# Performance work log

Hardware: AMD Instinct MI355X
Metric: run time of the kernel (lower is better)

Reference implementation:

```python
import jax, jax.numpy as jnp
import numpy as np

N_NODES = 100000

def setup_inputs() -> dict:
    key = jax.random.key(0)
    k1, k2 = jax.random.split(key)
    x = jax.random.normal(k1, (N_NODES, 48), dtype=jnp.float32)
    edge_index = jax.random.randint(k2, (2, 1600000), 0, N_NODES, dtype=jnp.int64)
    return {"x": x, "edge_index": edge_index}

def reference(x, edge_index):
    # adj = SparseTensor.from_edge_index(edge_index): row=edge_index[0], col=edge_index[1]
    # adj.matmul(x): out[i] = sum over edges with row==i of x[col]
    row, col = edge_index[0], edge_index[1]
    x_neighbors_sum = jax.ops.segment_sum(x[col], row, num_segments=x.shape[0])  # [N, D]
    node_labels = jnp.concatenate((x, x_neighbors_sum), axis=-1)  # [N, 2D]
    return node_labels
```

## Files before the change

kernel.cpp:

```cpp
#include <hip/hip_runtime.h>


constexpr int D_IN  = 48;
constexpr int BSH   = 7;
constexpr int BNODES = 1 << BSH;
constexpr int MAXNB = 1024;
constexpr int CAPB  = 2400;
constexpr int OVF_MAX = 4096;

constexpr int PT_THREADS = 256;
constexpr int PT_ITEMS   = 32;
constexpr int PT_TILE    = PT_THREADS * PT_ITEMS;

constexpr int AG_THREADS = 512;
constexpr int AG_ITEMS   = 5;


__device__ __forceinline__ unsigned int bf16rne(float f) {
    unsigned int u = __float_as_uint(f);
    return (u + 0x7fffu + ((u >> 16) & 1u)) >> 16;
}
__device__ __forceinline__ unsigned int packbf(float a, float b) {
    return bf16rne(a) | (bf16rne(b) << 16);
}
__device__ __forceinline__ void accbf(float4& a, uint2 u) {
    a.x += __uint_as_float(u.x << 16);
    a.y += __uint_as_float(u.x & 0xffff0000u);
    a.z += __uint_as_float(u.y << 16);
    a.w += __uint_as_float(u.y & 0xffff0000u);
}
__device__ __forceinline__ void add4(float4& a, const float4& b) {
    a.x += b.x; a.y += b.y; a.z += b.z; a.w += b.w;
}


__global__ __launch_bounds__(PT_THREADS)
void prep_kernel(const int* __restrict__ row, const int* __restrict__ col,
                 int* __restrict__ gcursor, unsigned int* __restrict__ pairs,
                 int* __restrict__ ovf_cnt, uint2* __restrict__ ovf,
                 const float4* __restrict__ x4, uint4* __restrict__ x2u4,
                 float4* __restrict__ out4,
                 int n_edges, int nb, int ntiles, int n_nodes) {
    __shared__ int hist[MAXNB];
    __shared__ int offs[MAXNB];
    __shared__ int gbase[MAXNB];
    __shared__ int wsum[PT_THREADS / 64];

    int t = threadIdx.x;

    if (blockIdx.x >= ntiles) {
        int i = (blockIdx.x - ntiles) * PT_THREADS + t;
        if (i < n_nodes * 6) {
            int n = i / 6, s = i - n * 6;
            float4 v0 = x4[(size_t)n * 12 + 2 * s];
            float4 v1 = x4[(size_t)n * 12 + 2 * s + 1];
            out4[(size_t)n * 24 + 2 * s]     = v0;
            out4[(size_t)n * 24 + 2 * s + 1] = v1;
            x2u4[(size_t)n * 6 + s] =
                make_uint4(packbf(v0.x, v0.y), packbf(v0.z, v0.w),
                           packbf(v1.x, v1.y), packbf(v1.z, v1.w));
        }
        return;
    }

    int tile0 = blockIdx.x * PT_TILE;

    for (int i = t; i < nb; i += PT_THREADS) hist[i] = 0;
    __syncthreads();

#pragma unroll 8
    for (int j = 0; j < PT_ITEMS; ++j) {
        int e = tile0 + j * PT_THREADS + t;
        if (e < n_edges) atomicAdd(&hist[row[e] >> BSH], 1);
    }
    __syncthreads();

    int cb = t * 4;
    int loc[4];
    int s = 0;
#pragma unroll
    for (int j = 0; j < 4; ++j) {
        int i = cb + j;
        loc[j] = (i < nb) ? hist[i] : 0;
        s += loc[j];
    }
    int sc = s;
#pragma unroll
    for (int o = 1; o < 64; o <<= 1) {
        int u = __shfl_up(sc, o);
        if ((t & 63) >= o) sc += u;
    }
    if ((t & 63) == 63) wsum[t >> 6] = sc;
    __syncthreads();
    int wpre = 0;
#pragma unroll
    for (int w = 0; w < PT_THREADS / 64; ++w)
        if (w < (t >> 6)) wpre += wsum[w];
    int run = wpre + sc - s;
#pragma unroll
    for (int j = 0; j < 4; ++j) {
        int i = cb + j;
        if (i < nb) { offs[i] = run; run += loc[j]; }
    }
    __syncthreads();

    for (int i = t; i < nb; i += PT_THREADS) {
        int cnt = hist[i];
        gbase[i] = cnt ? (atomicAdd(&gcursor[i], cnt) - offs[i]) : 0;
        hist[i] = offs[i];
    }
    __syncthreads();

#pragma unroll 8
    for (int j = 0; j < PT_ITEMS; ++j) {
        int e = tile0 + j * PT_THREADS + t;
        if (e < n_edges) {
            int r = row[e], c = col[e];
            int b = r >> BSH;
            int lpos = atomicAdd(&hist[b], 1);
            int g = gbase[b] + lpos;
            if (g < CAPB) {
                pairs[(size_t)b * CAPB + g] =
                    ((unsigned int)(r & (BNODES - 1)) << 17) | (unsigned int)c;
            } else {
                int o = atomicAdd(ovf_cnt, 1);
                if (o < OVF_MAX)
                    ovf[o] = make_uint2((unsigned int)r, (unsigned int)c);
            }
        }
    }
}


template <int USE_BF16>
__global__ __launch_bounds__(AG_THREADS)
void agg_kernel(const float4* __restrict__ x4, const uint2* __restrict__ xbv,
                const unsigned int* __restrict__ pairs,
                const int* __restrict__ gcursor,
                const int* __restrict__ ovf_cnt, const uint2* __restrict__ ovf,
                float4* __restrict__ out4, int n_nodes) {
    __shared__ unsigned int scol[CAPB];
    __shared__ int hist[BNODES];
    __shared__ int offs[BNODES];
    __shared__ int cur[BNODES];
    __shared__ int perm[BNODES];
    __shared__ int dh[64];
    __shared__ int dcur[64];
    __shared__ int wtot;

    int t   = threadIdx.x;
    int bkt = blockIdx.x;
    int cnt = min(gcursor[bkt], CAPB);
    const unsigned int* pb = pairs + (size_t)bkt * CAPB;

    if (t < BNODES) hist[t] = 0;
    if (t < 64) dh[t] = 0;
    __syncthreads();

    unsigned int pv[AG_ITEMS];
#pragma unroll
    for (int j = 0; j < AG_ITEMS; ++j) {
        int idx = t + j * AG_THREADS;
        if (idx < cnt) {
            pv[j] = pb[idx];
            atomicAdd(&hist[pv[j] >> 17], 1);
        }
    }
    __syncthreads();

    int v = (t < BNODES) ? hist[t] : 0;
    int sc = v;
#pragma unroll
    for (int o = 1; o < 64; o <<= 1) {
        int u = __shfl_up(sc, o);
        if ((t & 63) >= o) sc += u;
    }
    if (t == 63) wtot = sc;
    if (t < BNODES) atomicAdd(&dh[min(v, 63)], 1);
    __syncthreads();
    if (t < BNODES) {
        int excl = sc - v + ((t >= 64) ? wtot : 0);
        offs[t] = excl;
        cur[t]  = excl;
    }
    {
        int dv = (t < 64) ? dh[t] : 0;
        int dsc = dv;
#pragma unroll
        for (int o = 1; o < 64; o <<= 1) {
            int u = __shfl_up(dsc, o);
            if ((t & 63) >= o) dsc += u;
        }
        if (t < 64) dcur[t] = dsc - dv;
    }
    __syncthreads();

#pragma unroll
    for (int j = 0; j < AG_ITEMS; ++j) {
        int idx = t + j * AG_THREADS;
        if (idx < cnt) {
            int pos = atomicAdd(&cur[pv[j] >> 17], 1);
            scol[pos] = pv[j] & 0x1FFFFu;
        }
    }
    if (t < BNODES) {
        int slot = atomicAdd(&dcur[min(hist[t], 63)], 1);
        perm[slot] = t;
    }
    __syncthreads();

    int n  = perm[t >> 2];
    int qt = t & 3;
    float4 a0 = make_float4(0.f, 0.f, 0.f, 0.f);
    float4 a1 = make_float4(0.f, 0.f, 0.f, 0.f);
    float4 a2 = make_float4(0.f, 0.f, 0.f, 0.f);

    int k0 = offs[n];
    int k1 = k0 + hist[n];
    int k  = k0;
    if constexpr (USE_BF16) {
        for (; k + 2 <= k1; k += 2) {
            const uint2* pA = xbv + (size_t)scol[k]     * 12 + qt * 3;
            const uint2* pB = xbv + (size_t)scol[k + 1] * 12 + qt * 3;
            uint2 A0 = pA[0], A1 = pA[1], A2 = pA[2];
            uint2 B0 = pB[0], B1 = pB[1], B2 = pB[2];
            accbf(a0, A0); accbf(a1, A1); accbf(a2, A2);
            accbf(a0, B0); accbf(a1, B1); accbf(a2, B2);
        }
        if (k < k1) {
            const uint2* p0 = xbv + (size_t)scol[k] * 12 + qt * 3;
            accbf(a0, p0[0]); accbf(a1, p0[1]); accbf(a2, p0[2]);
        }
    } else {
        for (; k + 2 <= k1; k += 2) {
            size_t c0 = (size_t)scol[k]     * 12 + qt * 3;
            size_t c1 = (size_t)scol[k + 1] * 12 + qt * 3;
            float4 u0 = x4[c0], u1 = x4[c0 + 1], u2 = x4[c0 + 2];
            float4 w0 = x4[c1], w1 = x4[c1 + 1], w2 = x4[c1 + 2];
            add4(a0, u0); add4(a1, u1); add4(a2, u2);
            add4(a0, w0); add4(a1, w1); add4(a2, w2);
        }
        if (k < k1) {
            size_t c0 = (size_t)scol[k] * 12 + qt * 3;
            add4(a0, x4[c0]); add4(a1, x4[c0 + 1]); add4(a2, x4[c0 + 2]);
        }
    }

    int oc = min(*ovf_cnt, OVF_MAX);
    for (int i = 0; i < oc; ++i) {
        uint2 rc = ovf[i];
        if ((int)(rc.x >> BSH) == bkt && (int)(rc.x & (BNODES - 1)) == n) {
            const float4* xr = x4 + (size_t)rc.y * 12 + qt * 3;
            add4(a0, xr[0]); add4(a1, xr[1]); add4(a2, xr[2]);
        }
    }

    int node = (bkt << BSH) + n;
    if (node < n_nodes) {
        size_t ob = (size_t)node * 24;
        out4[ob + 12 + qt * 3 + 0] = a0;
        out4[ob + 12 + qt * 3 + 1] = a1;
        out4[ob + 12 + qt * 3 + 2] = a2;
        if constexpr (!USE_BF16) {
            size_t xb = (size_t)node * 12;
            out4[ob + qt * 3 + 0] = x4[xb + qt * 3 + 0];
            out4[ob + qt * 3 + 1] = x4[xb + qt * 3 + 1];
            out4[ob + qt * 3 + 2] = x4[xb + qt * 3 + 2];
        }
    }
}


__global__ void init_out_kernel(const float4* __restrict__ x4,
                                float4* __restrict__ out4, int n_nodes) {
    int idx = blockIdx.x * blockDim.x + threadIdx.x;
    int total = n_nodes * 24;
    if (idx >= total) return;
    int i = idx / 24;
    int q = idx - i * 24;
    out4[idx] = (q < 12) ? x4[i * 12 + q] : make_float4(0.f, 0.f, 0.f, 0.f);
}

__global__ void scatter_add_kernel(const float* __restrict__ x,
                                   const int* __restrict__ row,
                                   const int* __restrict__ col,
                                   float* __restrict__ out, int n_edges) {
    long long gid = (long long)blockIdx.x * blockDim.x + threadIdx.x;
    long long total = (long long)n_edges * D_IN;
    if (gid >= total) return;
    int e = (int)(gid / D_IN);
    int d = (int)(gid - (long long)e * D_IN);
    atomicAdd(out + (long long)row[e] * 96 + D_IN + d,
              x[(long long)col[e] * D_IN + d]);
}


extern "C" void kernel_launch(void* const* d_in, const int* in_sizes, int n_in,
                              void* d_out, int out_size, void* d_ws, size_t ws_size,
                              hipStream_t stream) {
    const float* x  = (const float*)d_in[0];
    const int*   ei = (const int*)d_in[1];
    float*       out = (float*)d_out;

    int n_nodes = in_sizes[0] / D_IN;
    int n_edges = in_sizes[1] / 2;
    const int* row = ei;
    const int* col = ei + n_edges;

    int nb = (n_nodes + BNODES - 1) >> BSH;
    int ntiles = (n_edges + PT_TILE - 1) / PT_TILE;
    bool col_fits = n_nodes <= (1 << 17);

    size_t t2_bytes = ((size_t)nb * CAPB + nb + 1 + 2 * (size_t)OVF_MAX) * 4;
    size_t x2_off   = (t2_bytes + 15) & ~(size_t)15;
    size_t t1_bytes = x2_off + (size_t)n_nodes * 96;

    if (nb > MAXNB || !col_fits || ws_size < t2_bytes) {
        int init_total = n_nodes * 24;
        init_out_kernel<<<(init_total + 255) / 256, 256, 0, stream>>>(
            (const float4*)x, (float4*)out, n_nodes);
        long long total = (long long)n_edges * D_IN;
        scatter_add_kernel<<<(int)((total + 255) / 256), 256, 0, stream>>>(
            x, row, col, out, n_edges);
        return;
    }

    unsigned int* pairs = (unsigned int*)d_ws;
    int* gcursor = (int*)(pairs + (size_t)nb * CAPB);
    int* ovf_cnt = gcursor + nb;
    uint2* ovf   = (uint2*)(ovf_cnt + 1);
    bool bf16_tier = (ws_size >= t1_bytes);
    uint4* x2u4  = (uint4*)((char*)d_ws + x2_off);

    hipMemsetAsync(gcursor, 0, (size_t)(nb + 1) * sizeof(int), stream);

    int conv_blocks = bf16_tier ? (n_nodes * 6 + PT_THREADS - 1) / PT_THREADS : 0;
    prep_kernel<<<ntiles + conv_blocks, PT_THREADS, 0, stream>>>(
        row, col, gcursor, pairs, ovf_cnt, ovf,
        (const float4*)x, x2u4, (float4*)out, n_edges, nb, ntiles, n_nodes);

    if (bf16_tier) {
        agg_kernel<1><<<nb, AG_THREADS, 0, stream>>>(
            (const float4*)x, (const uint2*)x2u4, pairs, gcursor,
            ovf_cnt, ovf, (float4*)out, n_nodes);
    } else {
        agg_kernel<0><<<nb, AG_THREADS, 0, stream>>>(
            (const float4*)x, nullptr, pairs, gcursor,
            ovf_cnt, ovf, (float4*)out, n_nodes);
    }
}
```

Before: 87.71 us.

## Split bucket cursors and pair storage into per-XCD segments

```diff
diff --git a/kernel.cpp b/kernel.cpp
--- a/kernel.cpp
+++ b/kernel.cpp
@@ -5,15 +5,16 @@
 constexpr int BSH   = 7;
 constexpr int BNODES = 1 << BSH;
 constexpr int MAXNB = 1024;
-constexpr int CAPB  = 2400;
+constexpr int NXCD  = 8;
+constexpr int CAPS  = 352;
 constexpr int OVF_MAX = 4096;
 
 constexpr int PT_THREADS = 256;
-constexpr int PT_ITEMS   = 32;
+constexpr int PT_ITEMS   = 16;
 constexpr int PT_TILE    = PT_THREADS * PT_ITEMS;
 
 constexpr int AG_THREADS = 512;
-constexpr int AG_ITEMS   = 5;
+constexpr int SCOL_CAP   = NXCD * CAPS;
 
 
 __device__ __forceinline__ unsigned int bf16rne(float f) {
@@ -64,14 +65,22 @@
     }
 
     int tile0 = blockIdx.x * PT_TILE;
+    int xcd   = blockIdx.x & (NXCD - 1);
 
     for (int i = t; i < nb; i += PT_THREADS) hist[i] = 0;
     __syncthreads();
 
-#pragma unroll 8
+    int r[PT_ITEMS], c[PT_ITEMS];
+#pragma unroll
     for (int j = 0; j < PT_ITEMS; ++j) {
         int e = tile0 + j * PT_THREADS + t;
-        if (e < n_edges) atomicAdd(&hist[row[e] >> BSH], 1);
+        if (e < n_edges) {
+            r[j] = row[e];
+            c[j] = col[e];
+            atomicAdd(&hist[r[j] >> BSH], 1);
+        } else {
+            r[j] = -1;
+        }
     }
     __syncthreads();
 
@@ -106,26 +115,24 @@
 
     for (int i = t; i < nb; i += PT_THREADS) {
         int cnt = hist[i];
-        gbase[i] = cnt ? (atomicAdd(&gcursor[i], cnt) - offs[i]) : 0;
+        gbase[i] = cnt ? (atomicAdd(&gcursor[xcd * nb + i], cnt) - offs[i]) : 0;
         hist[i] = offs[i];
     }
     __syncthreads();
 
-#pragma unroll 8
+#pragma unroll
     for (int j = 0; j < PT_ITEMS; ++j) {
-        int e = tile0 + j * PT_THREADS + t;
-        if (e < n_edges) {
-            int r = row[e], c = col[e];
-            int b = r >> BSH;
+        if (r[j] >= 0) {
+            int b = r[j] >> BSH;
             int lpos = atomicAdd(&hist[b], 1);
             int g = gbase[b] + lpos;
-            if (g < CAPB) {
-                pairs[(size_t)b * CAPB + g] =
-                    ((unsigned int)(r & (BNODES - 1)) << 17) | (unsigned int)c;
+            if (g < CAPS) {
+                pairs[(size_t)(xcd * nb + b) * CAPS + g] =
+                    ((unsigned int)(r[j] & (BNODES - 1)) << 17) | (unsigned int)c[j];
             } else {
                 int o = atomicAdd(ovf_cnt, 1);
                 if (o < OVF_MAX)
-                    ovf[o] = make_uint2((unsigned int)r, (unsigned int)c);
+                    ovf[o] = make_uint2((unsigned int)r[j], (unsigned int)c[j]);
             }
         }
     }
@@ -138,8 +145,8 @@
                 const unsigned int* __restrict__ pairs,
                 const int* __restrict__ gcursor,
                 const int* __restrict__ ovf_cnt, const uint2* __restrict__ ovf,
-                float4* __restrict__ out4, int n_nodes) {
-    __shared__ unsigned int scol[CAPB];
+                float4* __restrict__ out4, int n_nodes, int nb) {
+    __shared__ unsigned int scol[SCOL_CAP];
     __shared__ int hist[BNODES];
     __shared__ int offs[BNODES];
     __shared__ int cur[BNODES];
@@ -150,20 +157,19 @@
 
     int t   = threadIdx.x;
     int bkt = blockIdx.x;
-    int cnt = min(gcursor[bkt], CAPB);
-    const unsigned int* pb = pairs + (size_t)bkt * CAPB;
 
     if (t < BNODES) hist[t] = 0;
     if (t < 64) dh[t] = 0;
     __syncthreads();
 
-    unsigned int pv[AG_ITEMS];
-#pragma unroll
-    for (int j = 0; j < AG_ITEMS; ++j) {
-        int idx = t + j * AG_THREADS;
-        if (idx < cnt) {
-            pv[j] = pb[idx];
-            atomicAdd(&hist[pv[j] >> 17], 1);
+    unsigned int pv[NXCD];
+#pragma unroll
+    for (int sseg = 0; sseg < NXCD; ++sseg) {
+        int cs = min(gcursor[sseg * nb + bkt], CAPS);
+        pv[sseg] = 0xFFFFFFFFu;
+        if (t < cs) {
+            pv[sseg] = pairs[(size_t)(sseg * nb + bkt) * CAPS + t];
+            atomicAdd(&hist[pv[sseg] >> 17], 1);
         }
     }
     __syncthreads();
@@ -196,11 +202,10 @@
     __syncthreads();
 
 #pragma unroll
-    for (int j = 0; j < AG_ITEMS; ++j) {
-        int idx = t + j * AG_THREADS;
-        if (idx < cnt) {
-            int pos = atomicAdd(&cur[pv[j] >> 17], 1);
-            scol[pos] = pv[j] & 0x1FFFFu;
+    for (int sseg = 0; sseg < NXCD; ++sseg) {
+        if (pv[sseg] != 0xFFFFFFFFu) {
+            int pos = atomicAdd(&cur[pv[sseg] >> 17], 1);
+            scol[pos] = pv[sseg] & 0x1FFFFu;
         }
     }
     if (t < BNODES) {
@@ -311,7 +316,8 @@
     int ntiles = (n_edges + PT_TILE - 1) / PT_TILE;
     bool col_fits = n_nodes <= (1 << 17);
 
-    size_t t2_bytes = ((size_t)nb * CAPB + nb + 1 + 2 * (size_t)OVF_MAX) * 4;
+    size_t t2_bytes = ((size_t)NXCD * nb * CAPS + (size_t)NXCD * nb + 1 +
+                       2 * (size_t)OVF_MAX) * 4;
     size_t x2_off   = (t2_bytes + 15) & ~(size_t)15;
     size_t t1_bytes = x2_off + (size_t)n_nodes * 96;
 
@@ -326,13 +332,13 @@
     }
 
     unsigned int* pairs = (unsigned int*)d_ws;
-    int* gcursor = (int*)(pairs + (size_t)nb * CAPB);
-    int* ovf_cnt = gcursor + nb;
+    int* gcursor = (int*)(pairs + (size_t)NXCD * nb * CAPS);
+    int* ovf_cnt = gcursor + (size_t)NXCD * nb;
     uint2* ovf   = (uint2*)(ovf_cnt + 1);
     bool bf16_tier = (ws_size >= t1_bytes);
     uint4* x2u4  = (uint4*)((char*)d_ws + x2_off);
 
-    hipMemsetAsync(gcursor, 0, (size_t)(nb + 1) * sizeof(int), stream);
+    hipMemsetAsync(gcursor, 0, ((size_t)NXCD * nb + 1) * sizeof(int), stream);
 
     int conv_blocks = bf16_tier ? (n_nodes * 6 + PT_THREADS - 1) / PT_THREADS : 0;
     prep_kernel<<<ntiles + conv_blocks, PT_THREADS, 0, stream>>>(
@@ -342,10 +348,10 @@
     if (bf16_tier) {
         agg_kernel<1><<<nb, AG_THREADS, 0, stream>>>(
             (const float4*)x, (const uint2*)x2u4, pairs, gcursor,
-            ovf_cnt, ovf, (float4*)out, n_nodes);
+            ovf_cnt, ovf, (float4*)out, n_nodes, nb);
     } else {
         agg_kernel<0><<<nb, AG_THREADS, 0, stream>>>(
             (const float4*)x, nullptr, pairs, gcursor,
-            ovf_cnt, ovf, (float4*)out, n_nodes);
-    }
-}
+            ovf_cnt, ovf, (float4*)out, n_nodes, nb);
+    }
+}
```

Result: faster. 79.05 us (-9.9%).
